# Performance work log

Hardware: AMD Instinct MI355X
Metric: run time of the kernel (lower is better)

## Reference

```python
import jax, jax.numpy as jnp
import numpy as np

N_NODES = 100000
N_EDGES = 600000
D_IN = 128
HID = 128
N_LAYERS = 3


def gcn_conv(x, W, b, src, dst, num_nodes):
    """PyG-style GCNConv: D^{-1/2}(A+I)D^{-1/2} X W + b (self-loops added)."""
    h = x @ W  # [N, H]
    # in-degree including self-loop
    deg = jnp.zeros((num_nodes,), dtype=x.dtype).at[dst].add(1.0) + 1.0
    dinv = jax.lax.rsqrt(deg)
    norm = dinv[src] * dinv[dst]  # [E]
    msg = h[src] * norm[:, None]  # [E, H] gather + scale
    out = jax.ops.segment_sum(msg, dst, num_segments=num_nodes)  # scatter-add
    out = out + h * (1.0 / deg)[:, None]  # self-loop term (norm = 1/deg)
    return out + b


def setup_inputs() -> dict:
    key = jax.random.key(0)
    ks = jax.random.split(key, 16)
    x = jax.random.normal(ks[0], (N_NODES, D_IN), dtype=jnp.float32)
    edge_index = jax.random.randint(ks[1], (2, N_EDGES), 0, N_NODES, dtype=jnp.int64)
    timestamp = jax.random.uniform(ks[2], (1,), dtype=jnp.float32)
    # GCN layer weights (glorot-ish scale) and biases
    def glorot(k, fan_in, fan_out):
        s = jnp.sqrt(6.0 / (fan_in + fan_out))
        return jax.random.uniform(k, (fan_in, fan_out), minval=-s, maxval=s, dtype=jnp.float32)
    W_gcn = [glorot(ks[3], D_IN, HID), glorot(ks[4], HID, HID), glorot(ks[5], HID, HID)]
    b_gcn = [jnp.zeros((HID,), jnp.float32) for _ in range(N_LAYERS)]
    # temporal gate MLP: Linear(1,H) -> tanh -> Linear(H,H) -> sigmoid
    Wg1 = glorot(ks[6], 1, HID)
    bg1 = jnp.zeros((HID,), jnp.float32)
    Wg2 = glorot(ks[7], HID, HID)
    bg2 = jnp.zeros((HID,), jnp.float32)
    return {
        "x": x, "edge_index": edge_index, "timestamp": timestamp,
        "W0": W_gcn[0], "b0": b_gcn[0],
        "W1": W_gcn[1], "b1": b_gcn[1],
        "W2": W_gcn[2], "b2": b_gcn[2],
        "Wg1": Wg1, "bg1": bg1, "Wg2": Wg2, "bg2": bg2,
    }


def reference(x, edge_index, timestamp, W0, b0, W1, b1, W2, b2, Wg1, bg1, Wg2, bg2):
    src, dst = edge_index[0], edge_index[1]
    num_nodes = x.shape[0]
    # temporal gate: [1,1] -> [1,H], broadcast over nodes
    t = timestamp.reshape(1, 1)
    gate = jax.nn.sigmoid(jnp.tanh(t @ Wg1 + bg1) @ Wg2 + bg2)  # [1, H]
    for (W, b) in ((W0, b0), (W1, b1), (W2, b2)):
        x = gcn_conv(x, W, b, src, dst, num_nodes)
        x = jax.nn.relu(x)
        x = x * gate  # broadcast gate over nodes
        # dropout: identity in eval mode
    return x
```

## Files before the change

kernel.cpp:

```cpp
#include <hip/hip_runtime.h>
#include <hip/hip_bf16.h>
#include <hip/hip_fp16.h>
#include <math.h>


#define D 128

typedef __attribute__((ext_vector_type(8))) short short8;
typedef __attribute__((ext_vector_type(8))) _Float16 half8;
typedef __attribute__((ext_vector_type(4))) float floatx4;

__device__ __forceinline__ unsigned bf16_rne(float x) {
    unsigned u = __float_as_uint(x);
    return (u + 0x7FFFu + ((u >> 16) & 1u)) >> 16;
}

__device__ __forceinline__ void gload_lds16(const void* g, void* l) {
    __builtin_amdgcn_global_load_lds(
        (const __attribute__((address_space(1))) unsigned int*)g,
        (__attribute__((address_space(3))) unsigned int*)l, 16, 0, 0);
}

__device__ __forceinline__ float h2f(unsigned short u) {
    return __half2float(__ushort_as_half(u));
}

__global__ __launch_bounds__(256) void prep_kernel(
    const int* __restrict__ w, int* __restrict__ src32,
    int* __restrict__ dst32, int* __restrict__ counts, int E,
    const float* __restrict__ W0, const float* __restrict__ W1,
    const float* __restrict__ W2, short8* __restrict__ Wf_hi,
    short8* __restrict__ Wf_lo,
    const float* __restrict__ t, const float* __restrict__ Wg1,
    const float* __restrict__ bg1, const float* __restrict__ Wg2,
    const float* __restrict__ bg2, float* __restrict__ gate)
{
    int b = blockIdx.x;
    if (b < 24) {
        int f = b * 256 + threadIdx.x;
        int layer = f >> 11;
        int fi = f & 2047;
        int lane = fi & 63;
        int tt = fi >> 6;
        int kc = tt >> 3, n = tt & 7;
        const float* W = (layer == 0) ? W0 : (layer == 1) ? W1 : W2;
        int krow = kc * 32 + (lane >> 4) * 8;
        int col = n * 16 + (lane & 15);
        short8 hv, lv;
        if (layer == 0) {
            #pragma unroll
            for (int j = 0; j < 8; j++) {
                float x = W[(size_t)(krow + j) * D + col];
                unsigned hb = bf16_rne(x);
                float hf = __uint_as_float(hb << 16);
                unsigned lb = bf16_rne(x - hf);
                hv[j] = (short)hb;
                lv[j] = (short)lb;
            }
        } else {
            #pragma unroll
            for (int j = 0; j < 8; j++) {
                float x = W[(size_t)(krow + j) * D + col];
                __half hh = __float2half(x);
                float hf = __half2float(hh);
                __half ll = __float2half(x - hf);
                hv[j] = (short)__half_as_ushort(hh);
                lv[j] = (short)__half_as_ushort(ll);
            }
        }
        Wf_hi[f] = hv;
        Wf_lo[f] = lv;
        return;
    }
    if (b == 24) {
        __shared__ float u[D];
        int j = threadIdx.x;
        if (j < D) {
            float tv = t[0];
            u[j] = tanhf(tv * Wg1[j] + bg1[j]);
        }
        __syncthreads();
        if (j < D) {
            float s = bg2[j];
            #pragma unroll 8
            for (int k = 0; k < D; k++) s += u[k] * Wg2[k * D + j];
            gate[j] = 1.0f / (1.0f + expf(-s));
        }
        return;
    }
    __shared__ int flag;
    if (threadIdx.x == 0) {
        int z = 0;
        for (int k = 0; k < 64; k++) z |= w[2 * k + 1];
        flag = (z == 0) ? 1 : 0;
    }
    __syncthreads();
    int i64 = flag;
    int e = (b - 25) * 256 + threadIdx.x;
    if (e >= E) return;
    int s = i64 ? w[2 * e] : w[e];
    int d = i64 ? w[2 * (E + e)] : w[E + e];
    src32[e] = s;
    dst32[e] = d;
    atomicAdd(&counts[d], 1);
}

#define SCHUNK 1024
__device__ __forceinline__ int cap4(int c) { return (c + 3) & ~3; }

__global__ __launch_bounds__(256) void scan_partial_kernel(
    const int* __restrict__ counts, int* __restrict__ bsums, int N)
{
    int base = blockIdx.x * SCHUNK + threadIdx.x * 4;
    int s = 0;
    if (base + 3 < N) {
        int4 v = *(const int4*)(counts + base);
        s = cap4(v.x) + cap4(v.y) + cap4(v.z) + cap4(v.w);
    } else {
        for (int k = 0; k < 4; k++) if (base + k < N) s += cap4(counts[base + k]);
    }
    #pragma unroll
    for (int off = 1; off < 64; off <<= 1) s += __shfl_xor(s, off);
    __shared__ int wsum[4];
    int lane = threadIdx.x & 63, wid = threadIdx.x >> 6;
    if (lane == 0) wsum[wid] = s;
    __syncthreads();
    if (threadIdx.x == 0)
        bsums[blockIdx.x] = wsum[0] + wsum[1] + wsum[2] + wsum[3];
}

__global__ __launch_bounds__(1024) void scan_bsums_kernel(
    int* __restrict__ bsums, int* __restrict__ total_out, int B)
{
    int t = threadIdx.x;
    int v = (t < B) ? bsums[t] : 0;
    int lane = t & 63, wid = t >> 6;
    int s = v;
    #pragma unroll
    for (int off = 1; off < 64; off <<= 1) {
        int n = __shfl_up(s, off);
        if (lane >= off) s += n;
    }
    __shared__ int wsum[16], wpre[16];
    if (lane == 63) wsum[wid] = s;
    __syncthreads();
    if (t < 16) {
        int ws = wsum[t];
        #pragma unroll
        for (int off = 1; off < 16; off <<= 1) {
            int n = __shfl_up(ws, off);
            if (t >= off) ws += n;
        }
        wpre[t] = ws;
    }
    __syncthreads();
    int wex = wid ? wpre[wid - 1] : 0;
    if (t < B) bsums[t] = wex + (s - v);
    if (t == 0) *total_out = wpre[15];
}

__global__ __launch_bounds__(256) void scan_final_kernel(
    const int* __restrict__ counts, const int* __restrict__ bsums,
    int* __restrict__ offsets, int* __restrict__ cursor,
    float* __restrict__ dinv, int N)
{
    int base = blockIdx.x * SCHUNK + threadIdx.x * 4;
    int c[4];
    float dd[4];
    bool full = (base + 3 < N);
    if (full) {
        int4 v = *(const int4*)(counts + base);
        c[0] = cap4(v.x); c[1] = cap4(v.y); c[2] = cap4(v.z); c[3] = cap4(v.w);
        dd[0] = rsqrtf((float)(v.x + 1)); dd[1] = rsqrtf((float)(v.y + 1));
        dd[2] = rsqrtf((float)(v.z + 1)); dd[3] = rsqrtf((float)(v.w + 1));
    } else {
        for (int k = 0; k < 4; k++) {
            int r = (base + k < N) ? counts[base + k] : 0;
            c[k] = (base + k < N) ? cap4(r) : 0;
            dd[k] = rsqrtf((float)(r + 1));
        }
    }
    int sum = c[0] + c[1] + c[2] + c[3];
    int lane = threadIdx.x & 63, wid = threadIdx.x >> 6;
    int s = sum;
    #pragma unroll
    for (int off = 1; off < 64; off <<= 1) {
        int n = __shfl_up(s, off);
        if (lane >= off) s += n;
    }
    __shared__ int wsum[4], wpre[4];
    if (lane == 63) wsum[wid] = s;
    __syncthreads();
    if (threadIdx.x == 0) {
        int a = 0;
        #pragma unroll
        for (int k = 0; k < 4; k++) { wpre[k] = a; a += wsum[k]; }
    }
    __syncthreads();
    int e0 = bsums[blockIdx.x] + wpre[wid] + (s - sum);
    int4 o = make_int4(e0, e0 + c[0], e0 + c[0] + c[1], e0 + c[0] + c[1] + c[2]);
    float4 dv = make_float4(dd[0], dd[1], dd[2], dd[3]);
    if (full) {
        *(int4*)(offsets + base) = o;
        *(int4*)(cursor + base) = o;
        *(float4*)(dinv + base) = dv;
    } else {
        int oo[4] = { o.x, o.y, o.z, o.w };
        for (int k = 0; k < 4; k++)
            if (base + k < N) {
                offsets[base + k] = oo[k];
                cursor[base + k] = oo[k];
                dinv[base + k] = dd[k];
            }
    }
}

__global__ __launch_bounds__(256) void bucket_kernel(
    const int* __restrict__ src32, const int* __restrict__ dst32,
    int* __restrict__ cursor, int* __restrict__ edges4, int E)
{
    int e = blockIdx.x * blockDim.x + threadIdx.x;
    if (e >= E) return;
    int s = src32[e];
    int d = dst32[e];
    int pos = atomicAdd(&cursor[d], 1);
    edges4[pos] = s;
}

__global__ __launch_bounds__(256) void expand_kernel(
    const int* __restrict__ edges4, const float* __restrict__ dinv,
    int2* __restrict__ edges8, int cap)
{
    int i = blockIdx.x * blockDim.x + threadIdx.x;
    if (i >= cap) return;
    int s = edges4[i];
    int ss = (s < 0) ? 0 : s;
    float f = (s < 0) ? 0.f : dinv[ss];
    edges8[i] = make_int2(ss, __float_as_int(f));
}

#define WSTAGE(kc_)                                                           \
    {                                                                         \
        short* wb_ = Wfs + (((kc_) & 1) ? 8192 : 0);                          \
        const short8* gh_ = Wf_hi + (size_t)(kc_) * 512;                      \
        const short8* gl_ = Wf_lo + (size_t)(kc_) * 512;                      \
        _Pragma("unroll")                                                     \
        for (int i_ = 0; i_ < 2; i_++) {                                      \
            int c_ = i_ * 256 + w * 64;                                       \
            gload_lds16(gh_ + c_ + lane, wb_ + c_ * 8);                       \
            gload_lds16(gl_ + c_ + lane, wb_ + 4096 + c_ * 8);                \
        }                                                                     \
    }

#define MFMA_BLOCK(kc)                                                        \
    {                                                                         \
        const short* wb = Wfs + (((kc) & 1) ? 8192 : 0);                      \
        _Pragma("unroll")                                                     \
        for (int n = 0; n < 8; n++) {                                         \
            short8 bh = *(const short8*)(wb + (n * 64 + lane) * 8);           \
            short8 bl = *(const short8*)(wb + 4096 + (n * 64 + lane) * 8);    \
            acc[0][n] = __builtin_amdgcn_mfma_f32_16x16x32_bf16(ah0, bh, acc[0][n], 0, 0, 0); \
            acc[0][n] = __builtin_amdgcn_mfma_f32_16x16x32_bf16(ah0, bl, acc[0][n], 0, 0, 0); \
            acc[0][n] = __builtin_amdgcn_mfma_f32_16x16x32_bf16(al0, bh, acc[0][n], 0, 0, 0); \
            acc[1][n] = __builtin_amdgcn_mfma_f32_16x16x32_bf16(ah1, bh, acc[1][n], 0, 0, 0); \
            acc[1][n] = __builtin_amdgcn_mfma_f32_16x16x32_bf16(ah1, bl, acc[1][n], 0, 0, 0); \
            acc[1][n] = __builtin_amdgcn_mfma_f32_16x16x32_bf16(al1, bh, acc[1][n], 0, 0, 0); \
        }                                                                     \
    }

#define MFMA_BLOCK_F16(kc)                                                    \
    {                                                                         \
        const short* wb = Wfs + (((kc) & 1) ? 8192 : 0);                      \
        _Pragma("unroll")                                                     \
        for (int n = 0; n < 8; n++) {                                         \
            half8 bh = *(const half8*)(wb + (n * 64 + lane) * 8);             \
            half8 bl = *(const half8*)(wb + 4096 + (n * 64 + lane) * 8);      \
            acc[0][n] = __builtin_amdgcn_mfma_f32_16x16x32_f16(ah0, bh, acc[0][n], 0, 0, 0); \
            acc[0][n] = __builtin_amdgcn_mfma_f32_16x16x32_f16(ah0, bl, acc[0][n], 0, 0, 0); \
            acc[1][n] = __builtin_amdgcn_mfma_f32_16x16x32_f16(ah1, bh, acc[1][n], 0, 0, 0); \
            acc[1][n] = __builtin_amdgcn_mfma_f32_16x16x32_f16(ah1, bl, acc[1][n], 0, 0, 0); \
        }                                                                     \
    }

#define EPILOGUE()                                                            \
    _Pragma("unroll")                                                         \
    for (int rt = 0; rt < 2; rt++) {                                          \
        _Pragma("unroll")                                                     \
        for (int reg = 0; reg < 4; reg++) {                                   \
            int row = rowbase + rt * 16 + qd * 4 + reg;                       \
            if (row < M) {                                                    \
                unsigned short* hp = H16 + (size_t)row * D + m16;             \
                _Pragma("unroll")                                             \
                for (int n = 0; n < 8; n++)                                   \
                    hp[n * 16] = __half_as_ushort(__float2half(acc[rt][n][reg])); \
            }                                                                 \
        }                                                                     \
    }

#define GBM 128
__device__ __forceinline__ void cvt8(const float* f, short8& hi, short8& lo) {
    #pragma unroll
    for (int j = 0; j < 8; j++) {
        unsigned hb = bf16_rne(f[j]);
        float hf = __uint_as_float(hb << 16);
        unsigned lb = bf16_rne(f[j] - hf);
        hi[j] = (short)hb;
        lo[j] = (short)lb;
    }
}

__global__ __launch_bounds__(256) void gemm_f32_kernel(
    const float* __restrict__ X, const short8* __restrict__ Wf_hi,
    const short8* __restrict__ Wf_lo, unsigned short* __restrict__ H16, int M)
{
    __shared__ short Wfs[16384];
    int tid = threadIdx.x;
    int w = tid >> 6, lane = tid & 63;
    int m16 = lane & 15, qd = lane >> 4;
    int rowbase = blockIdx.x * GBM + w * 32;

    int r0 = rowbase + m16;      if (r0 >= M) r0 = M - 1;
    int r1 = rowbase + m16 + 16; if (r1 >= M) r1 = M - 1;
    const float* xp0 = X + (size_t)r0 * D + qd * 8;
    const float* xp1 = X + (size_t)r1 * D + qd * 8;

    floatx4 acc[2][8];
    #pragma unroll
    for (int rt = 0; rt < 2; rt++)
        #pragma unroll
        for (int n = 0; n < 8; n++)
            acc[rt][n] = (floatx4)(0.f);

    #define LOADA(kc_, A0, A1)                                              \
        {                                                                   \
            *(float4*)(A0)     = *(const float4*)(xp0 + (kc_) * 32);        \
            *(float4*)(A0 + 4) = *(const float4*)(xp0 + (kc_) * 32 + 4);    \
            *(float4*)(A1)     = *(const float4*)(xp1 + (kc_) * 32);        \
            *(float4*)(A1 + 4) = *(const float4*)(xp1 + (kc_) * 32 + 4);    \
        }

    float a0c[8], a1c[8], a0n[8], a1n[8];
    WSTAGE(0)
    LOADA(0, a0c, a1c)

    #pragma unroll
    for (int kc = 0; kc < 4; kc++) {
        __syncthreads();
        if (kc < 3) {
            WSTAGE(kc + 1)
            LOADA(kc + 1, a0n, a1n)
        }
        short8 ah0, al0, ah1, al1;
        cvt8(a0c, ah0, al0);
        cvt8(a1c, ah1, al1);
        MFMA_BLOCK(kc)
        if (kc < 3) {
            #pragma unroll
            for (int z = 0; z < 8; z++) { a0c[z] = a0n[z]; a1c[z] = a1n[z]; }
        }
    }
    #undef LOADA
    EPILOGUE()
}

__global__ __launch_bounds__(256) void gemm_f16_kernel(
    const unsigned short* __restrict__ Xh,
    const short8* __restrict__ Wf_hi, const short8* __restrict__ Wf_lo,
    unsigned short* __restrict__ H16, int M)
{
    __shared__ short Wfs[16384];
    int tid = threadIdx.x;
    int w = tid >> 6, lane = tid & 63;
    int m16 = lane & 15, qd = lane >> 4;
    int rowbase = blockIdx.x * GBM + w * 32;

    int r0 = rowbase + m16;      if (r0 >= M) r0 = M - 1;
    int r1 = rowbase + m16 + 16; if (r1 >= M) r1 = M - 1;
    const unsigned short* xh0 = Xh + (size_t)r0 * D + qd * 8;
    const unsigned short* xh1 = Xh + (size_t)r1 * D + qd * 8;

    floatx4 acc[2][8];
    #pragma unroll
    for (int rt = 0; rt < 2; rt++)
        #pragma unroll
        for (int n = 0; n < 8; n++)
            acc[rt][n] = (floatx4)(0.f);

    half8 ah0, ah1, nh0, nh1;
    WSTAGE(0)
    ah0 = *(const half8*)(xh0);
    ah1 = *(const half8*)(xh1);

    #pragma unroll
    for (int kc = 0; kc < 4; kc++) {
        __syncthreads();
        if (kc < 3) {
            WSTAGE(kc + 1)
            nh0 = *(const half8*)(xh0 + (kc + 1) * 32);
            nh1 = *(const half8*)(xh1 + (kc + 1) * 32);
        }
        MFMA_BLOCK_F16(kc)
        if (kc < 3) { ah0 = nh0; ah1 = nh1; }
    }
    EPILOGUE()
}

__global__ __launch_bounds__(256) void agg_kernel(
    const unsigned short* __restrict__ H16, const int2* __restrict__ edges,
    const int* __restrict__ offsets, const float* __restrict__ dinv,
    const float* __restrict__ bias, const float* __restrict__ gate,
    float* __restrict__ outF, unsigned short* __restrict__ outH,
    int M, int writeF32)
{
    int t = threadIdx.x;
    int hw = t >> 5;
    int l32 = t & 31;
    int node = blockIdx.x * 8 + hw;
    if (node >= M) return;

    int beg = offsets[node];
    int end = offsets[node + 1];
    float dv = dinv[node];
    const unsigned short* __restrict__ Hc = H16 + l32 * 4;
    ushort4 us = *(const ushort4*)(Hc + (size_t)node * D);
    float4 acc = make_float4(0.f, 0.f, 0.f, 0.f);

    int4 p0 = make_int4(0, 0, 0, 0), p1 = make_int4(0, 0, 0, 0);
    if (beg < end) {
        p0 = *(const int4*)(edges + beg);
        p1 = *(const int4*)(edges + beg + 2);
    }
    for (int j = beg; j < end; j += 4) {
        int jn = j + 4;
        int jp = (jn < end) ? jn : beg;
        int4 q0 = *(const int4*)(edges + jp);
        int4 q1 = *(const int4*)(edges + jp + 2);
        ushort4 u0 = *(const ushort4*)(Hc + (size_t)p0.x * D);
        ushort4 u1 = *(const ushort4*)(Hc + (size_t)p0.z * D);
        ushort4 u2 = *(const ushort4*)(Hc + (size_t)p1.x * D);
        ushort4 u3 = *(const ushort4*)(Hc + (size_t)p1.z * D);
        float n0 = __int_as_float(p0.y) * dv, n1 = __int_as_float(p0.w) * dv;
        float n2 = __int_as_float(p1.y) * dv, n3 = __int_as_float(p1.w) * dv;
        acc.x = fmaf(h2f(u3.x), n3, fmaf(h2f(u2.x), n2, fmaf(h2f(u1.x), n1, fmaf(h2f(u0.x), n0, acc.x))));
        acc.y = fmaf(h2f(u3.y), n3, fmaf(h2f(u2.y), n2, fmaf(h2f(u1.y), n1, fmaf(h2f(u0.y), n0, acc.y))));
        acc.z = fmaf(h2f(u3.z), n3, fmaf(h2f(u2.z), n2, fmaf(h2f(u1.z), n1, fmaf(h2f(u0.z), n0, acc.z))));
        acc.w = fmaf(h2f(u3.w), n3, fmaf(h2f(u2.w), n2, fmaf(h2f(u1.w), n1, fmaf(h2f(u0.w), n0, acc.w))));
        p0 = q0; p1 = q1;
    }

    float nself = dv * dv;
    acc.x = fmaf(h2f(us.x), nself, acc.x);
    acc.y = fmaf(h2f(us.y), nself, acc.y);
    acc.z = fmaf(h2f(us.z), nself, acc.z);
    acc.w = fmaf(h2f(us.w), nself, acc.w);

    float4 bv = *(const float4*)(bias + l32 * 4);
    float4 gv = *(const float4*)(gate + l32 * 4);
    acc.x = fmaxf(acc.x + bv.x, 0.f) * gv.x;
    acc.y = fmaxf(acc.y + bv.y, 0.f) * gv.y;
    acc.z = fmaxf(acc.z + bv.z, 0.f) * gv.z;
    acc.w = fmaxf(acc.w + bv.w, 0.f) * gv.w;

    if (writeF32) {
        *(float4*)(outF + (size_t)node * D + l32 * 4) = acc;
    } else {
        ushort4 hs = make_ushort4(
            __half_as_ushort(__float2half(acc.x)),
            __half_as_ushort(__float2half(acc.y)),
            __half_as_ushort(__float2half(acc.z)),
            __half_as_ushort(__float2half(acc.w)));
        *(ushort4*)(outH + (size_t)node * D + l32 * 4) = hs;
    }
}

static inline size_t align_up(size_t v, size_t a) { return (v + a - 1) & ~(a - 1); }

extern "C" void kernel_launch(void* const* d_in, const int* in_sizes, int n_in,
                              void* d_out, int out_size, void* d_ws, size_t ws_size,
                              hipStream_t stream)
{
    const float* x   = (const float*)d_in[0];
    const int*   ei  = (const int*)d_in[1];
    const float* ts  = (const float*)d_in[2];
    const float* Wl[3] = { (const float*)d_in[3], (const float*)d_in[5], (const float*)d_in[7] };
    const float* bl[3] = { (const float*)d_in[4], (const float*)d_in[6], (const float*)d_in[8] };
    const float* Wg1 = (const float*)d_in[9];
    const float* bg1 = (const float*)d_in[10];
    const float* Wg2 = (const float*)d_in[11];
    const float* bg2 = (const float*)d_in[12];

    const int N = in_sizes[0] / D;
    const int E = in_sizes[1] / 2;
    const int NB = (N + SCHUNK - 1) / SCHUNK;
    const size_t ECAP = (size_t)E + 3 * (size_t)N;

    char* p = (char*)d_ws;
    unsigned short* h16 = (unsigned short*)p; p += align_up((size_t)N * D * 2, 256);
    unsigned short* xh  = (unsigned short*)p; p += align_up((size_t)N * D * 2, 256);
    int* src32  = (int*)p;   p += align_up((size_t)E * 4, 256);
    int* dst32  = (int*)p;   p += align_up((size_t)E * 4, 256);
    int* counts = (int*)p;   p += align_up((size_t)N * 4, 256);
    float* dinv = (float*)p; p += align_up((size_t)N * 4, 256);
    int* offs   = (int*)p;   p += align_up((size_t)(N + 1) * 4, 256);
    int* cursor = (int*)p;   p += align_up((size_t)N * 4, 256);
    int* edges4 = (int*)p;   p += align_up(ECAP * 4, 256);
    int2* edges8 = (int2*)p; p += align_up(ECAP * 8, 256);
    float* gate = (float*)p; p += align_up((size_t)D * 4, 256);
    int* bsums  = (int*)p;   p += align_up((size_t)NB * 4, 256);
    short8* Wf_hi = (short8*)p; p += align_up((size_t)3 * 2048 * 16, 256);
    short8* Wf_lo = (short8*)p; p += align_up((size_t)3 * 2048 * 16, 256);
    (void)ws_size; (void)n_in; (void)out_size;

    (void)hipMemsetAsync(counts, 0, (size_t)N * 4, stream);
    (void)hipMemsetAsync(edges4, 0xFF, ECAP * 4, stream);

    int egrid = (E + 255) / 256;
    prep_kernel<<<25 + egrid, 256, 0, stream>>>(
        ei, src32, dst32, counts, E,
        Wl[0], Wl[1], Wl[2], Wf_hi, Wf_lo,
        ts, Wg1, bg1, Wg2, bg2, gate);
    scan_partial_kernel<<<NB, 256, 0, stream>>>(counts, bsums, N);
    scan_bsums_kernel<<<1, 1024, 0, stream>>>(bsums, offs + N, NB);
    scan_final_kernel<<<NB, 256, 0, stream>>>(counts, bsums, offs, cursor, dinv, N);
    bucket_kernel<<<egrid, 256, 0, stream>>>(src32, dst32, cursor, edges4, E);
    int xgrid = (int)((ECAP + 255) / 256);
    expand_kernel<<<xgrid, 256, 0, stream>>>(edges4, dinv, edges8, (int)ECAP);

    int ggrid = (N + GBM - 1) / GBM;
    int agrid = (N + 7) / 8;
    gemm_f32_kernel<<<ggrid, 256, 0, stream>>>(x, Wf_hi, Wf_lo, h16, N);
    agg_kernel<<<agrid, 256, 0, stream>>>(h16, edges8, offs, dinv, bl[0], gate,
                                          nullptr, xh, N, 0);
    gemm_f16_kernel<<<ggrid, 256, 0, stream>>>(xh, Wf_hi + 2048, Wf_lo + 2048, h16, N);
    agg_kernel<<<agrid, 256, 0, stream>>>(h16, edges8, offs, dinv, bl[1], gate,
                                          nullptr, xh, N, 0);
    gemm_f16_kernel<<<ggrid, 256, 0, stream>>>(xh, Wf_hi + 4096, Wf_lo + 4096, h16, N);
    agg_kernel<<<agrid, 256, 0, stream>>>(h16, edges8, offs, dinv, bl[2], gate,
                                          (float*)d_out, nullptr, N, 1);
}
```

Before: 240.8 us.

## Fuse edge expand into bucketing and deepen gather prefetch in aggregation

The bucket kernel now looks up dinv[src] and writes the (src, dinv) pair straight into the CSR edge array. This removes the separate expand kernel and the intermediate int edge buffer, and the padding slots are zero-filled by memset. The aggregation loop is also software-pipelined one step deeper: it prefetches edge indices two groups ahead and the H rows of the next group before computing the current one. The cost is more registers per thread and some redundant loads of the fallback group at the loop tail.

```diff
diff --git a/kernel.cpp b/kernel.cpp
--- a/kernel.cpp
+++ b/kernel.cpp
@@ -217,26 +217,16 @@
 
 __global__ __launch_bounds__(256) void bucket_kernel(
     const int* __restrict__ src32, const int* __restrict__ dst32,
-    int* __restrict__ cursor, int* __restrict__ edges4, int E)
+    const float* __restrict__ dinv, int* __restrict__ cursor,
+    int2* __restrict__ edges8, int E)
 {
     int e = blockIdx.x * blockDim.x + threadIdx.x;
     if (e >= E) return;
     int s = src32[e];
     int d = dst32[e];
+    float f = dinv[s];
     int pos = atomicAdd(&cursor[d], 1);
-    edges4[pos] = s;
-}
-
-__global__ __launch_bounds__(256) void expand_kernel(
-    const int* __restrict__ edges4, const float* __restrict__ dinv,
-    int2* __restrict__ edges8, int cap)
-{
-    int i = blockIdx.x * blockDim.x + threadIdx.x;
-    if (i >= cap) return;
-    int s = edges4[i];
-    int ss = (s < 0) ? 0 : s;
-    float f = (s < 0) ? 0.f : dinv[ss];
-    edges8[i] = make_int2(ss, __float_as_int(f));
+    edges8[pos] = make_int2(s, __float_as_int(f));
 }
 
 #define WSTAGE(kc_)                                                           \
@@ -425,27 +415,35 @@
     ushort4 us = *(const ushort4*)(Hc + (size_t)node * D);
     float4 acc = make_float4(0.f, 0.f, 0.f, 0.f);
 
-    int4 p0 = make_int4(0, 0, 0, 0), p1 = make_int4(0, 0, 0, 0);
     if (beg < end) {
-        p0 = *(const int4*)(edges + beg);
-        p1 = *(const int4*)(edges + beg + 2);
-    }
-    for (int j = beg; j < end; j += 4) {
-        int jn = j + 4;
-        int jp = (jn < end) ? jn : beg;
-        int4 q0 = *(const int4*)(edges + jp);
-        int4 q1 = *(const int4*)(edges + jp + 2);
+        int4 p0 = *(const int4*)(edges + beg);
+        int4 p1 = *(const int4*)(edges + beg + 2);
         ushort4 u0 = *(const ushort4*)(Hc + (size_t)p0.x * D);
         ushort4 u1 = *(const ushort4*)(Hc + (size_t)p0.z * D);
         ushort4 u2 = *(const ushort4*)(Hc + (size_t)p1.x * D);
         ushort4 u3 = *(const ushort4*)(Hc + (size_t)p1.z * D);
-        float n0 = __int_as_float(p0.y) * dv, n1 = __int_as_float(p0.w) * dv;
-        float n2 = __int_as_float(p1.y) * dv, n3 = __int_as_float(p1.w) * dv;
-        acc.x = fmaf(h2f(u3.x), n3, fmaf(h2f(u2.x), n2, fmaf(h2f(u1.x), n1, fmaf(h2f(u0.x), n0, acc.x))));
-        acc.y = fmaf(h2f(u3.y), n3, fmaf(h2f(u2.y), n2, fmaf(h2f(u1.y), n1, fmaf(h2f(u0.y), n0, acc.y))));
-        acc.z = fmaf(h2f(u3.z), n3, fmaf(h2f(u2.z), n2, fmaf(h2f(u1.z), n1, fmaf(h2f(u0.z), n0, acc.z))));
-        acc.w = fmaf(h2f(u3.w), n3, fmaf(h2f(u2.w), n2, fmaf(h2f(u1.w), n1, fmaf(h2f(u0.w), n0, acc.w))));
-        p0 = q0; p1 = q1;
+        int j1 = (beg + 4 < end) ? beg + 4 : beg;
+        int4 q0 = *(const int4*)(edges + j1);
+        int4 q1 = *(const int4*)(edges + j1 + 2);
+
+        for (int j = beg; j < end; j += 4) {
+            int jn = j + 8;
+            int jp = (jn < end) ? jn : beg;
+            int4 r0 = *(const int4*)(edges + jp);
+            int4 r1 = *(const int4*)(edges + jp + 2);
+            ushort4 v0 = *(const ushort4*)(Hc + (size_t)q0.x * D);
+            ushort4 v1 = *(const ushort4*)(Hc + (size_t)q0.z * D);
+            ushort4 v2 = *(const ushort4*)(Hc + (size_t)q1.x * D);
+            ushort4 v3 = *(const ushort4*)(Hc + (size_t)q1.z * D);
+            float n0 = __int_as_float(p0.y) * dv, n1 = __int_as_float(p0.w) * dv;
+            float n2 = __int_as_float(p1.y) * dv, n3 = __int_as_float(p1.w) * dv;
+            acc.x = fmaf(h2f(u3.x), n3, fmaf(h2f(u2.x), n2, fmaf(h2f(u1.x), n1, fmaf(h2f(u0.x), n0, acc.x))));
+            acc.y = fmaf(h2f(u3.y), n3, fmaf(h2f(u2.y), n2, fmaf(h2f(u1.y), n1, fmaf(h2f(u0.y), n0, acc.y))));
+            acc.z = fmaf(h2f(u3.z), n3, fmaf(h2f(u2.z), n2, fmaf(h2f(u1.z), n1, fmaf(h2f(u0.z), n0, acc.z))));
+            acc.w = fmaf(h2f(u3.w), n3, fmaf(h2f(u2.w), n2, fmaf(h2f(u1.w), n1, fmaf(h2f(u0.w), n0, acc.w))));
+            p0 = q0; p1 = q1; q0 = r0; q1 = r1;
+            u0 = v0; u1 = v1; u2 = v2; u3 = v3;
+        }
     }
 
     float nself = dv * dv;
@@ -503,7 +501,6 @@
     float* dinv = (float*)p; p += align_up((size_t)N * 4, 256);
     int* offs   = (int*)p;   p += align_up((size_t)(N + 1) * 4, 256);
     int* cursor = (int*)p;   p += align_up((size_t)N * 4, 256);
-    int* edges4 = (int*)p;   p += align_up(ECAP * 4, 256);
     int2* edges8 = (int2*)p; p += align_up(ECAP * 8, 256);
     float* gate = (float*)p; p += align_up((size_t)D * 4, 256);
     int* bsums  = (int*)p;   p += align_up((size_t)NB * 4, 256);
@@ -512,7 +509,7 @@
     (void)ws_size; (void)n_in; (void)out_size;
 
     (void)hipMemsetAsync(counts, 0, (size_t)N * 4, stream);
-    (void)hipMemsetAsync(edges4, 0xFF, ECAP * 4, stream);
+    (void)hipMemsetAsync(edges8, 0, ECAP * 8, stream);
 
     int egrid = (E + 255) / 256;
     prep_kernel<<<25 + egrid, 256, 0, stream>>>(
@@ -522,9 +519,7 @@
     scan_partial_kernel<<<NB, 256, 0, stream>>>(counts, bsums, N);
     scan_bsums_kernel<<<1, 1024, 0, stream>>>(bsums, offs + N, NB);
     scan_final_kernel<<<NB, 256, 0, stream>>>(counts, bsums, offs, cursor, dinv, N);
-    bucket_kernel<<<egrid, 256, 0, stream>>>(src32, dst32, cursor, edges4, E);
-    int xgrid = (int)((ECAP + 255) / 256);
-    expand_kernel<<<xgrid, 256, 0, stream>>>(edges4, dinv, edges8, (int)ECAP);
+    bucket_kernel<<<egrid, 256, 0, stream>>>(src32, dst32, dinv, cursor, edges8, E);
 
     int ggrid = (N + GBM - 1) / GBM;
     int agrid = (N + 7) / 8;
```

Result: no change. 237.5 us (-1.4%).
